# Optimization experiments

Hardware: AMD Instinct MI355X
Metric: run time of the kernel (lower is better)

Reference implementation:

```python
import jax, jax.numpy as jnp
import numpy as np

N_SIGMA = 2
N_CLASS = 8
FG_WEIGHT = jnp.array([10., 10., 10., 40., 80., 100., 60., 20.], dtype=jnp.float32)
W_INST, W_VAR, W_SEED = 1.0, 10.0, 1.0
MIN_PIXELS = 128


def lovasz_hinge_flat(logits, labels):
    # logits, labels: [P] flat; labels in {0,1}
    signs = 2.0 * labels - 1.0
    errors = 1.0 - logits * signs
    order = jnp.argsort(-errors)  # descending
    errors_sorted = errors[order]
    gt_sorted = labels[order]
    gts = gt_sorted.sum()
    inter = gts - jnp.cumsum(gt_sorted)
    union = gts + jnp.cumsum(1.0 - gt_sorted)
    jac = 1.0 - inter / union
    grad = jnp.concatenate([jac[:1], jac[1:] - jac[:-1]])
    return jnp.dot(jax.nn.relu(errors_sorted), jax.lax.stop_gradient(grad))


def setup_inputs() -> dict:
    key = jax.random.key(0)
    k1, k2, k3, k4 = jax.random.split(key, 4)
    B, H, W, N = 2, 512, 1024, 8
    prediction = jax.random.normal(k1, (B, 12, H, W), dtype=jnp.float32)
    bbox = jax.random.randint(k2, (B, 9, H, W), 0, 2, dtype=jnp.int32)
    masks = jax.random.randint(k3, (B, N, H, W), 0, 2, dtype=jnp.int32)
    cls_ids = jax.random.randint(k4, (B, N), 0, 8, dtype=jnp.int32)
    return {"prediction": prediction, "bbox": bbox, "masks": masks, "cls_ids": cls_ids}


def _forward(prediction, bbox, masks, cls_ids):
    B, C, H, W = prediction.shape
    N = masks.shape[1]
    sg = jax.lax.stop_gradient
    # coordinate map: full 2048/1024 linspace sliced to [:W]/[:H], as in the buffer
    xm = jnp.linspace(0.0, 2.0, 2048, dtype=prediction.dtype)[:W]
    ym = jnp.linspace(0.0, 1.0, 1024, dtype=prediction.dtype)[:H]
    xym = jnp.stack([jnp.broadcast_to(xm[None, :], (H, W)),
                     jnp.broadcast_to(ym[:, None], (H, W))], axis=0)  # [2,H,W]

    spatial_emb = jnp.tanh(prediction[:, 0:2]) + xym[None]            # [B,2,H,W]
    sigma = prediction[:, 2:2 + N_SIGMA]                               # [B,2,H,W]
    seed = jax.nn.sigmoid(prediction[:, 2 + N_SIGMA:2 + N_SIGMA + N_CLASS])  # [B,8,H,W]

    # background seed loss: sum over cls 1..8 of seed[cls-1]^2 where bbox[cls]==0
    bg = bbox[:, 1:9] == 0                                             # [B,8,H,W]
    seed_bg = jnp.sum(jnp.where(bg, seed * seed, 0.0), axis=(1, 2, 3))  # [B]

    m = (masks > 0).astype(prediction.dtype)                           # [B,N,H,W]
    cnt = m.sum(axis=(2, 3))                                           # [B,N]
    valid = (cnt >= MIN_PIXELS).astype(prediction.dtype)               # [B,N]
    cnt_safe = jnp.maximum(cnt, 1.0)

    # per-instance masked means (to_center=False -> center from spatial_emb)
    center = jnp.einsum('bnhw,bchw->bnc', m, spatial_emb) / cnt_safe[..., None]  # [B,N,2]
    s_mean = jnp.einsum('bnhw,bchw->bnc', m, sigma) / cnt_safe[..., None]        # [B,N,2]

    # var loss: mean over [n_sigma, P] of (sigma_in - s.detach())^2
    diff2 = (sigma[:, None] - sg(s_mean)[..., None, None]) ** 2        # [B,N,2,H,W]
    var_inst = jnp.einsum('bnchw,bnhw->bn', diff2, m) / (N_SIGMA * cnt_safe)

    s_exp = jnp.exp(s_mean * 10.0)                                     # [B,N,2]
    d2 = (spatial_emb[:, None] - center[..., None, None]) ** 2         # [B,N,2,H,W]
    dist = jnp.exp(-jnp.einsum('bnchw,bnc->bnhw', d2, s_exp))          # [B,N,H,W]

    # lovasz hinge per instance on dist*2-1 vs mask
    logits = (dist * 2.0 - 1.0).reshape(B * N, H * W)
    labels = m.reshape(B * N, H * W)
    lov = jax.vmap(lovasz_hinge_flat)(logits, labels).reshape(B, N)    # [B,N]

    # foreground seed loss
    seed_cls = jnp.take_along_axis(seed, cls_ids[..., None, None].astype(jnp.int32), axis=1)  # [B,N,H,W]
    fw = FG_WEIGHT[cls_ids]                                            # [B,N]
    seed_fg = fw * jnp.einsum('bnhw,bnhw->bn', m, (seed_cls - sg(dist)) ** 2)

    obj = valid.sum(axis=1)                                            # [B]
    obj_safe = jnp.maximum(obj, 1.0)
    inst_l = jnp.sum(lov * valid, axis=1) / obj_safe
    var_l = jnp.sum(var_inst * valid, axis=1) / obj_safe
    seed_l = (seed_bg + jnp.sum(seed_fg * valid, axis=1)) / (H * W)
    loss = jnp.mean(W_INST * inst_l + W_VAR * var_l + W_SEED * seed_l)
    return loss


def reference(prediction, bbox, masks, cls_ids):
    return _forward(prediction, bbox, masks, cls_ids)
```

## Files before the change

kernel.cpp:

```cpp
#include <hip/hip_runtime.h>
#include <cstdint>
#include <cstddef>

#define HW 524288
#define HW4 131072
#define NBIN 2048


__device__ __forceinline__ float wred(float v) {
#pragma unroll
  for (int o = 32; o > 0; o >>= 1) v += __shfl_xor(v, o, 64);
  return v;
}

__device__ __forceinline__ float fsig(float x) {
  return __builtin_amdgcn_rcpf(1.f + expf(-x));
}

__global__ __launch_bounds__(256) void pass1(
    const float* __restrict__ pred, const int* __restrict__ masks,
    double* __restrict__ acc)
{
  const int b = blockIdx.y;
  const int tid = threadIdx.x;
  const int g = blockIdx.x * 256 + tid;
  const float4* pb4 = (const float4*)(pred + (size_t)b * 12 * HW);
  const int4*   mk4 = (const int4*)(masks + (size_t)b * 8 * HW);

  int idx = g << 2;
  int h = idx >> 10, w = idx & 1023;
  float4 p0 = pb4[g];
  float4 p1 = pb4[HW4 + g];
  float4 s0 = pb4[2 * HW4 + g];
  float4 s1 = pb4[3 * HW4 + g];
  int4 mv[8];
#pragma unroll
  for (int n = 0; n < 8; n++) mv[n] = mk4[n * HW4 + g];

  float p0v[4] = {p0.x, p0.y, p0.z, p0.w}, p1v[4] = {p1.x, p1.y, p1.z, p1.w};
  float s0v[4] = {s0.x, s0.y, s0.z, s0.w}, s1v[4] = {s1.x, s1.y, s1.z, s1.w};
  float exv[4], eyv[4];
#pragma unroll
  for (int j = 0; j < 4; j++) {
    exv[j] = tanhf(p0v[j]) + (float)((w + j) * (2.0 / 2047.0));
    eyv[j] = tanhf(p1v[j]) + (float)(h * (1.0 / 1023.0));
  }

  float c[8] = {0}, cx[8] = {0}, cy[8] = {0}, sx[8] = {0}, sy[8] = {0},
        sxx[8] = {0}, syy[8] = {0};
#pragma unroll
  for (int n = 0; n < 8; n++) {
    int mvv[4] = {mv[n].x, mv[n].y, mv[n].z, mv[n].w};
#pragma unroll
    for (int j = 0; j < 4; j++) {
      float mf = (mvv[j] > 0) ? 1.f : 0.f;
      c[n] += mf; cx[n] += mf * exv[j]; cy[n] += mf * eyv[j];
      sx[n] += mf * s0v[j]; sy[n] += mf * s1v[j];
      sxx[n] += mf * s0v[j] * s0v[j]; syy[n] += mf * s1v[j] * s1v[j];
    }
  }

  __shared__ float red[4][56];
  int lane = tid & 63, wid = tid >> 6;
#pragma unroll
  for (int n = 0; n < 8; n++) {
    float r0 = wred(c[n]),  r1 = wred(cx[n]), r2 = wred(cy[n]),
          r3 = wred(sx[n]), r4 = wred(sy[n]), r5 = wred(sxx[n]),
          r6 = wred(syy[n]);
    if (lane == 0) {
      red[wid][n * 7 + 0] = r0; red[wid][n * 7 + 1] = r1;
      red[wid][n * 7 + 2] = r2; red[wid][n * 7 + 3] = r3;
      red[wid][n * 7 + 4] = r4; red[wid][n * 7 + 5] = r5;
      red[wid][n * 7 + 6] = r6;
    }
  }
  __syncthreads();
  if (tid < 56) {
    float s = red[0][tid] + red[1][tid] + red[2][tid] + red[3][tid];
    int n = tid / 7, q = tid % 7;
    atomicAdd(&acc[((size_t)b * 8 + n) * 8 + q], (double)s);
  }
}

__global__ __launch_bounds__(1024) void pass3(
    const float* __restrict__ pred, const int* __restrict__ bbox,
    const int* __restrict__ masks, const int* __restrict__ cls_ids,
    double* __restrict__ acc, double* __restrict__ seedbg,
    unsigned* __restrict__ ghist)
{
  const int seg = blockIdx.y;
  const int b = seg >> 3, n = seg & 7;
  const int tid = threadIdx.x;
  __shared__ unsigned hist[NBIN * 2];
  __shared__ float redf[16][2];
  for (int j = tid; j < NBIN * 2; j += 1024) hist[j] = 0;

  const double* a = acc + seg * 8;
  double cntd = a[0];
  double cs = cntd < 1.0 ? 1.0 : cntd;
  float cxv = (float)(a[1] / cs), cyv = (float)(a[2] / cs);
  float sex = expf((float)(a[3] / cs) * 10.f);
  float sey = expf((float)(a[4] / cs) * 10.f);
  int cls = cls_ids[b * 8 + n];
  const float4* pb4 = (const float4*)(pred + (size_t)b * 12 * HW);
  const float4* sp4 = pb4 + (size_t)(4 + cls) * HW4;
  const float4* sb4 = pb4 + (size_t)(4 + n) * HW4;
  const int4*   mp4 = (const int4*)(masks + (size_t)seg * HW);
  const int4*   bb4 = (const int4*)(bbox + (size_t)b * 9 * HW) + (1 + n) * HW4;
  __syncthreads();

  float sf = 0.f, sbg = 0.f;
  int gbase = blockIdx.x * 4096;
#pragma unroll
  for (int i = 0; i < 4; i++) {
    int g = gbase + i * 1024 + tid;
    int idx = g << 2;
    int h = idx >> 10, w = idx & 1023;
    float4 p0 = pb4[g];
    float4 p1 = pb4[HW4 + g];
    int4 mv = mp4[g];
    float4 sv = sp4[g];
    float4 sb = sb4[g];
    int4 bv = bb4[g];
    float p0v[4] = {p0.x, p0.y, p0.z, p0.w}, p1v[4] = {p1.x, p1.y, p1.z, p1.w};
    float svv[4] = {sv.x, sv.y, sv.z, sv.w}, sbv[4] = {sb.x, sb.y, sb.z, sb.w};
    int mvv[4] = {mv.x, mv.y, mv.z, mv.w}, bvv[4] = {bv.x, bv.y, bv.z, bv.w};
#pragma unroll
    for (int j = 0; j < 4; j++) {
      int m = (mvv[j] > 0) ? 1 : 0;
      float ex = tanhf(p0v[j]) + (float)((w + j) * (2.0 / 2047.0));
      float ey = tanhf(p1v[j]) + (float)(h * (1.0 / 1023.0));
      float dx = ex - cxv, dy = ey - cyv;
      float d = expf(-(dx * dx * sex + dy * dy * sey));
      float sg = fsig(svv[j]);
      float df = sg - d;
      sf += m ? df * df : 0.f;
      float sgb = fsig(sbv[j]);
      sbg += (bvv[j] == 0) ? sgb * sgb : 0.f;
      float e = m ? 2.f - 2.f * d : 2.f * d;
      int k = (int)(e * 1024.f); k = k > (NBIN - 1) ? (NBIN - 1) : k;
      atomicAdd(&hist[k * 2 + m], 1u);
    }
  }
  __syncthreads();

  unsigned* gh = ghist + (size_t)seg * NBIN * 2;
  for (int j = tid; j < NBIN * 2; j += 1024) {
    unsigned v = hist[j];
    if (v) atomicAdd(&gh[j], v);
  }

  float r0 = wred(sf), r1 = wred(sbg);
  int lane = tid & 63, wid = tid >> 6;
  if (lane == 0) { redf[wid][0] = r0; redf[wid][1] = r1; }
  __syncthreads();
  if (tid == 0) {
    float t = 0.f;
    for (int w2 = 0; w2 < 16; w2++) t += redf[w2][0];
    atomicAdd(&acc[seg * 8 + 7], (double)t);
  } else if (tid == 64) {
    float t = 0.f;
    for (int w2 = 0; w2 < 16; w2++) t += redf[w2][1];
    atomicAdd(&seedbg[b], (double)t);
  }
}

__global__ __launch_bounds__(256) void pass4(
    const unsigned* __restrict__ ghist, const double* __restrict__ acc,
    const double* __restrict__ seedbg, const int* __restrict__ cls_ids,
    float* __restrict__ lov, unsigned* __restrict__ ctr,
    float* __restrict__ out)
{
  const int seg = blockIdx.x;
  const int tid = threadIdx.x;
  const int lane = tid & 63, wid = tid >> 6;
  __shared__ __align__(16) unsigned lh[NBIN * 2];
  __shared__ unsigned wc[4], wp[4];
  __shared__ double sred[4];

  const uint4* gh4 = (const uint4*)(ghist + (size_t)seg * NBIN * 2);
#pragma unroll
  for (int i = 0; i < 4; i++)
    ((uint4*)lh)[i * 256 + tid] = gh4[i * 256 + tid];
  __syncthreads();

  double G = acc[seg * 8 + 0];

  unsigned cntT = 0, posT = 0;
#pragma unroll
  for (int i = 0; i < 8; i++) {
    int kk = (NBIN - 1) - tid * 8 - i;
    unsigned h0 = lh[2 * kk], h1 = lh[2 * kk + 1];
    cntT += h0 + h1; posT += h1;
  }
  unsigned ic = cntT, ip = posT;
  for (int o = 1; o < 64; o <<= 1) {
    unsigned yc = __shfl_up(ic, o, 64), yp = __shfl_up(ip, o, 64);
    if (lane >= o) { ic += yc; ip += yp; }
  }
  if (lane == 63) { wc[wid] = ic; wp[wid] = ip; }
  __syncthreads();
  unsigned oc = 0, op = 0;
  for (int w2 = 0; w2 < wid; w2++) { oc += wc[w2]; op += wp[w2]; }
  unsigned p = oc + ic - cntT, C = op + ip - posT;

  double S = 0.0;
#pragma unroll
  for (int i = 0; i < 8; i++) {
    int kk = (NBIN - 1) - tid * 8 - i;
    unsigned n1 = lh[2 * kk + 1], n0 = lh[2 * kk];
    double ec = (kk + 0.5) * (1.0 / 1024.0);
    if (n1) {
      S += (double)n1 * ec / (G + (double)(p - C));
      p += n1; C += n1;
    }
    if (n0) {
      double rem = G - (double)C;
      if (rem > 0.0) {
        double aa = G + (double)(p - C);
        S += ec * rem * (1.0 / aa - 1.0 / (aa + (double)n0));
      }
      p += n0;
    }
  }
#pragma unroll
  for (int o = 32; o > 0; o >>= 1) S += __shfl_xor(S, o, 64);
  if (lane == 0) sred[wid] = S;
  __syncthreads();

  if (tid == 0) {
    double St = sred[0] + sred[1] + sred[2] + sred[3];
    atomicExch(&lov[seg], (float)St);
    __threadfence();
    unsigned old = atomicAdd(ctr, 1u);
    if (old == 15u) {
      __threadfence();
      const float FG[8] = {10.f, 10.f, 10.f, 40.f, 80.f, 100.f, 60.f, 20.f};
      double total = 0.0;
      for (int b = 0; b < 2; b++) {
        double obj = 0, inst = 0, varl = 0, sfg = 0;
        for (int n = 0; n < 8; n++) {
          int s = b * 8 + n;
          const double* a = acc + s * 8;
          double cnt = a[0];
          double cs = cnt < 1.0 ? 1.0 : cnt;
          double smx = a[3] / cs, smy = a[4] / cs;
          double var = ((a[5] - cnt * smx * smx) + (a[6] - cnt * smy * smy)) /
                       (2.0 * cs);
          double v = (cnt >= 128.0) ? 1.0 : 0.0;
          double lv = (double)atomicAdd(&lov[s], 0.0f);
          obj += v;
          inst += lv * v;
          varl += var * v;
          sfg += (double)FG[cls_ids[s]] * a[7] * v;
        }
        double objs = obj < 1.0 ? 1.0 : obj;
        double seedl = (seedbg[b] + sfg) / (double)HW;
        total += inst / objs + 10.0 * (varl / objs) + seedl;
      }
      out[0] = (float)(0.5 * total);
    }
  }
}

extern "C" void kernel_launch(void* const* d_in, const int* in_sizes, int n_in,
                              void* d_out, int out_size, void* d_ws, size_t ws_size,
                              hipStream_t stream)
{
  (void)in_sizes; (void)n_in; (void)out_size; (void)ws_size;
  const float* pred  = (const float*)d_in[0];
  const int*   bbox  = (const int*)d_in[1];
  const int*   masks = (const int*)d_in[2];
  const int*   cls   = (const int*)d_in[3];

  char* ws = (char*)d_ws;
  double*   acc    = (double*)(ws + 0);
  double*   seedbg = (double*)(ws + 1024);
  float*    lov    = (float*)(ws + 1040);
  unsigned* ctr    = (unsigned*)(ws + 1104);
  unsigned* ghist  = (unsigned*)(ws + 4096);

  hipMemsetAsync(d_ws, 0, 266240, stream);
  pass1<<<dim3(512, 2), 256, 0, stream>>>(pred, masks, acc);
  pass3<<<dim3(32, 16), 1024, 0, stream>>>(pred, bbox, masks, cls, acc, seedbg, ghist);
  pass4<<<16, 256, 0, stream>>>(ghist, acc, seedbg, cls, lov, ctr, (float*)d_out);
}
```

Baseline: 186.7 us.

## Halve histogram bins, pack pos/neg counts, use fast exp/tanh, double pass1 work

Cuts the Lovasz histogram from 2048 to 1024 bins and packs the positive and negative counts into one 32-bit shared atomic (16 bits each). The global histogram is merged with 64-bit atomics, which halves the shared atomics and the memset size. It also swaps tanhf/expf for __expf-based fast approximations and has each pass1 thread process two float4 chunks instead of one. The coarser bins loosen the Lovasz approximation, and a 16-bit half could overflow if one block puts more than 65535 negatives into a single bin.

```diff
diff --git a/kernel.cpp b/kernel.cpp
--- a/kernel.cpp
+++ b/kernel.cpp
@@ -4,7 +4,7 @@
 
 #define HW 524288
 #define HW4 131072
-#define NBIN 2048
+#define NBIN 1024
 
 
 __device__ __forceinline__ float wred(float v) {
@@ -14,7 +14,10 @@
 }
 
 __device__ __forceinline__ float fsig(float x) {
-  return __builtin_amdgcn_rcpf(1.f + expf(-x));
+  return __builtin_amdgcn_rcpf(1.f + __expf(-x));
+}
+__device__ __forceinline__ float ftanh(float x) {
+  return 1.f - 2.f * __builtin_amdgcn_rcpf(__expf(2.f * x) + 1.f);
 }
 
 __global__ __launch_bounds__(256) void pass1(
@@ -23,40 +26,43 @@
 {
   const int b = blockIdx.y;
   const int tid = threadIdx.x;
-  const int g = blockIdx.x * 256 + tid;
   const float4* pb4 = (const float4*)(pred + (size_t)b * 12 * HW);
   const int4*   mk4 = (const int4*)(masks + (size_t)b * 8 * HW);
 
-  int idx = g << 2;
-  int h = idx >> 10, w = idx & 1023;
-  float4 p0 = pb4[g];
-  float4 p1 = pb4[HW4 + g];
-  float4 s0 = pb4[2 * HW4 + g];
-  float4 s1 = pb4[3 * HW4 + g];
-  int4 mv[8];
-#pragma unroll
-  for (int n = 0; n < 8; n++) mv[n] = mk4[n * HW4 + g];
-
-  float p0v[4] = {p0.x, p0.y, p0.z, p0.w}, p1v[4] = {p1.x, p1.y, p1.z, p1.w};
-  float s0v[4] = {s0.x, s0.y, s0.z, s0.w}, s1v[4] = {s1.x, s1.y, s1.z, s1.w};
-  float exv[4], eyv[4];
-#pragma unroll
-  for (int j = 0; j < 4; j++) {
-    exv[j] = tanhf(p0v[j]) + (float)((w + j) * (2.0 / 2047.0));
-    eyv[j] = tanhf(p1v[j]) + (float)(h * (1.0 / 1023.0));
-  }
-
   float c[8] = {0}, cx[8] = {0}, cy[8] = {0}, sx[8] = {0}, sy[8] = {0},
         sxx[8] = {0}, syy[8] = {0};
-#pragma unroll
-  for (int n = 0; n < 8; n++) {
-    int mvv[4] = {mv[n].x, mv[n].y, mv[n].z, mv[n].w};
+
+#pragma unroll
+  for (int k = 0; k < 2; k++) {
+    const int g = blockIdx.x * 512 + k * 256 + tid;
+    int idx = g << 2;
+    int h = idx >> 10, w = idx & 1023;
+    float4 p0 = pb4[g];
+    float4 p1 = pb4[HW4 + g];
+    float4 s0 = pb4[2 * HW4 + g];
+    float4 s1 = pb4[3 * HW4 + g];
+    int4 mv[8];
+#pragma unroll
+    for (int n = 0; n < 8; n++) mv[n] = mk4[n * HW4 + g];
+
+    float p0v[4] = {p0.x, p0.y, p0.z, p0.w}, p1v[4] = {p1.x, p1.y, p1.z, p1.w};
+    float s0v[4] = {s0.x, s0.y, s0.z, s0.w}, s1v[4] = {s1.x, s1.y, s1.z, s1.w};
+    float exv[4], eyv[4];
 #pragma unroll
     for (int j = 0; j < 4; j++) {
-      float mf = (mvv[j] > 0) ? 1.f : 0.f;
-      c[n] += mf; cx[n] += mf * exv[j]; cy[n] += mf * eyv[j];
-      sx[n] += mf * s0v[j]; sy[n] += mf * s1v[j];
-      sxx[n] += mf * s0v[j] * s0v[j]; syy[n] += mf * s1v[j] * s1v[j];
+      exv[j] = ftanh(p0v[j]) + (float)((w + j) * (2.0 / 2047.0));
+      eyv[j] = ftanh(p1v[j]) + (float)(h * (1.0 / 1023.0));
+    }
+#pragma unroll
+    for (int n = 0; n < 8; n++) {
+      int mvv[4] = {mv[n].x, mv[n].y, mv[n].z, mv[n].w};
+#pragma unroll
+      for (int j = 0; j < 4; j++) {
+        float mf = (mvv[j] > 0) ? 1.f : 0.f;
+        c[n] += mf; cx[n] += mf * exv[j]; cy[n] += mf * eyv[j];
+        sx[n] += mf * s0v[j]; sy[n] += mf * s1v[j];
+        sxx[n] += mf * s0v[j] * s0v[j]; syy[n] += mf * s1v[j] * s1v[j];
+      }
     }
   }
 
@@ -86,21 +92,21 @@
     const float* __restrict__ pred, const int* __restrict__ bbox,
     const int* __restrict__ masks, const int* __restrict__ cls_ids,
     double* __restrict__ acc, double* __restrict__ seedbg,
-    unsigned* __restrict__ ghist)
+    unsigned long long* __restrict__ ghist)
 {
   const int seg = blockIdx.y;
   const int b = seg >> 3, n = seg & 7;
   const int tid = threadIdx.x;
-  __shared__ unsigned hist[NBIN * 2];
+  __shared__ unsigned hist[NBIN];
   __shared__ float redf[16][2];
-  for (int j = tid; j < NBIN * 2; j += 1024) hist[j] = 0;
+  for (int j = tid; j < NBIN; j += 1024) hist[j] = 0;
 
   const double* a = acc + seg * 8;
   double cntd = a[0];
   double cs = cntd < 1.0 ? 1.0 : cntd;
   float cxv = (float)(a[1] / cs), cyv = (float)(a[2] / cs);
-  float sex = expf((float)(a[3] / cs) * 10.f);
-  float sey = expf((float)(a[4] / cs) * 10.f);
+  float sex = __expf((float)(a[3] / cs) * 10.f);
+  float sey = __expf((float)(a[4] / cs) * 10.f);
   int cls = cls_ids[b * 8 + n];
   const float4* pb4 = (const float4*)(pred + (size_t)b * 12 * HW);
   const float4* sp4 = pb4 + (size_t)(4 + cls) * HW4;
@@ -128,26 +134,27 @@
 #pragma unroll
     for (int j = 0; j < 4; j++) {
       int m = (mvv[j] > 0) ? 1 : 0;
-      float ex = tanhf(p0v[j]) + (float)((w + j) * (2.0 / 2047.0));
-      float ey = tanhf(p1v[j]) + (float)(h * (1.0 / 1023.0));
+      float ex = ftanh(p0v[j]) + (float)((w + j) * (2.0 / 2047.0));
+      float ey = ftanh(p1v[j]) + (float)(h * (1.0 / 1023.0));
       float dx = ex - cxv, dy = ey - cyv;
-      float d = expf(-(dx * dx * sex + dy * dy * sey));
-      float sg = fsig(svv[j]);
-      float df = sg - d;
+      float d = __expf(-(dx * dx * sex + dy * dy * sey));
+      float df = fsig(svv[j]) - d;
       sf += m ? df * df : 0.f;
       float sgb = fsig(sbv[j]);
       sbg += (bvv[j] == 0) ? sgb * sgb : 0.f;
       float e = m ? 2.f - 2.f * d : 2.f * d;
-      int k = (int)(e * 1024.f); k = k > (NBIN - 1) ? (NBIN - 1) : k;
-      atomicAdd(&hist[k * 2 + m], 1u);
-    }
-  }
-  __syncthreads();
-
-  unsigned* gh = ghist + (size_t)seg * NBIN * 2;
-  for (int j = tid; j < NBIN * 2; j += 1024) {
+      int k = (int)(e * 512.f); k = k > (NBIN - 1) ? (NBIN - 1) : k;
+      atomicAdd(&hist[k], m ? 65536u : 1u);
+    }
+  }
+  __syncthreads();
+
+  unsigned long long* gh = ghist + (size_t)seg * NBIN;
+  for (int j = tid; j < NBIN; j += 1024) {
     unsigned v = hist[j];
-    if (v) atomicAdd(&gh[j], v);
+    if (v)
+      atomicAdd(&gh[j], (unsigned long long)(v & 0xffffu) |
+                        ((unsigned long long)(v >> 16) << 32));
   }
 
   float r0 = wred(sf), r1 = wred(sbg);
@@ -166,7 +173,7 @@
 }
 
 __global__ __launch_bounds__(256) void pass4(
-    const unsigned* __restrict__ ghist, const double* __restrict__ acc,
+    const unsigned long long* __restrict__ ghist, const double* __restrict__ acc,
     const double* __restrict__ seedbg, const int* __restrict__ cls_ids,
     float* __restrict__ lov, unsigned* __restrict__ ctr,
     float* __restrict__ out)
@@ -178,9 +185,9 @@
   __shared__ unsigned wc[4], wp[4];
   __shared__ double sred[4];
 
-  const uint4* gh4 = (const uint4*)(ghist + (size_t)seg * NBIN * 2);
-#pragma unroll
-  for (int i = 0; i < 4; i++)
+  const uint4* gh4 = (const uint4*)(ghist + (size_t)seg * NBIN);
+#pragma unroll
+  for (int i = 0; i < 2; i++)
     ((uint4*)lh)[i * 256 + tid] = gh4[i * 256 + tid];
   __syncthreads();
 
@@ -188,8 +195,8 @@
 
   unsigned cntT = 0, posT = 0;
 #pragma unroll
-  for (int i = 0; i < 8; i++) {
-    int kk = (NBIN - 1) - tid * 8 - i;
+  for (int i = 0; i < 4; i++) {
+    int kk = (NBIN - 1) - tid * 4 - i;
     unsigned h0 = lh[2 * kk], h1 = lh[2 * kk + 1];
     cntT += h0 + h1; posT += h1;
   }
@@ -206,10 +213,10 @@
 
   double S = 0.0;
 #pragma unroll
-  for (int i = 0; i < 8; i++) {
-    int kk = (NBIN - 1) - tid * 8 - i;
+  for (int i = 0; i < 4; i++) {
+    int kk = (NBIN - 1) - tid * 4 - i;
     unsigned n1 = lh[2 * kk + 1], n0 = lh[2 * kk];
-    double ec = (kk + 0.5) * (1.0 / 1024.0);
+    double ec = (kk + 0.5) * (1.0 / 512.0);
     if (n1) {
       S += (double)n1 * ec / (G + (double)(p - C));
       p += n1; C += n1;
@@ -274,14 +281,14 @@
   const int*   cls   = (const int*)d_in[3];
 
   char* ws = (char*)d_ws;
-  double*   acc    = (double*)(ws + 0);
-  double*   seedbg = (double*)(ws + 1024);
-  float*    lov    = (float*)(ws + 1040);
-  unsigned* ctr    = (unsigned*)(ws + 1104);
-  unsigned* ghist  = (unsigned*)(ws + 4096);
-
-  hipMemsetAsync(d_ws, 0, 266240, stream);
-  pass1<<<dim3(512, 2), 256, 0, stream>>>(pred, masks, acc);
+  double*             acc    = (double*)(ws + 0);
+  double*             seedbg = (double*)(ws + 1024);
+  float*              lov    = (float*)(ws + 1040);
+  unsigned*           ctr    = (unsigned*)(ws + 1104);
+  unsigned long long* ghist  = (unsigned long long*)(ws + 4096);
+
+  hipMemsetAsync(d_ws, 0, 135168, stream);
+  pass1<<<dim3(256, 2), 256, 0, stream>>>(pred, masks, acc);
   pass3<<<dim3(32, 16), 1024, 0, stream>>>(pred, bbox, masks, cls, acc, seedbg, ghist);
   pass4<<<16, 256, 0, stream>>>(ghist, acc, seedbg, cls, lov, ctr, (float*)d_out);
 }
```

After: 171.5 us. 1.09x faster.
